# Kernel tuning notes

Hardware: AMD Instinct MI355X
Metric: run time of the kernel (lower is better)

Reference implementation:

```python
import jax, jax.numpy as jnp
import numpy as np

G, R, M, H, NH, OUT = 2048, 1024, 1024, 256, 8, 2
DH = H // NH


def _ln(x, g, b):
    m = jnp.mean(x, -1, keepdims=True)
    v = jnp.var(x, -1, keepdims=True)
    return (x - m) * jax.lax.rsqrt(v + 1e-5) * g + b


def _mha(xq, xkv, w, mask=None):
    # w: [4, H, H] = (Wq, Wk, Wv, Wo); mask: [Nq, Nk] bool (True = attend)
    q = (xq @ w[0]).reshape(-1, NH, DH)
    k = (xkv @ w[1]).reshape(-1, NH, DH)
    v = (xkv @ w[2]).reshape(-1, NH, DH)
    s = jnp.einsum('qhd,khd->hqk', q, k) * np.float32(1.0 / np.sqrt(DH))
    if mask is not None:
        s = jnp.where(mask[None], s, jnp.float32(-1e9))
    a = jax.nn.softmax(s, -1)
    ctx = jnp.einsum('hqk,khd->qhd', a, v).reshape(xq.shape[0], H)
    return ctx @ w[3]


def setup_inputs() -> dict:
    key = jax.random.key(0)
    ks = jax.random.split(key, 32)
    sc = np.float32(1.0 / np.sqrt(H))

    def n(i, shape, s=sc):
        return jax.random.normal(ks[i], shape, jnp.float32) * s

    inp = {}
    inp['gene_emb'] = n(0, (G, H), 0.02)
    inp['reaction_emb'] = n(1, (R, H), 0.02)
    inp['metab_emb'] = n(2, (M, H), 0.02)
    # PreProcessor (note: torch code reuses ONE LayerNorm instance -> shared params)
    inp['pre_w1'] = n(3, (H, H)); inp['pre_b1'] = jnp.zeros((H,), jnp.float32)
    inp['pre_w2'] = n(4, (H, H)); inp['pre_b2'] = jnp.zeros((H,), jnp.float32)
    inp['pre_ln_g'] = jnp.ones((H,), jnp.float32); inp['pre_ln_b'] = jnp.zeros((H,), jnp.float32)
    # NSA: 'M' block = masked attention per edge type (4), 'S' block = full self-attn per node type (3)
    inp['wm'] = n(5, (4, 4, H, H))
    inp['ws'] = n(6, (3, 4, H, H))
    inp['ln_g'] = jnp.ones((3, H), jnp.float32); inp['ln_b'] = jnp.zeros((3, H), jnp.float32)
    # AttentionalGraphAggregation
    inp['gate_w1'] = n(7, (H, H // 2)); inp['gate_b1'] = jnp.zeros((H // 2,), jnp.float32)
    inp['gate_w2'] = n(8, (H // 2, 1)); inp['gate_b2'] = jnp.zeros((1,), jnp.float32)
    inp['tr_w'] = n(9, (H, H)); inp['tr_b'] = jnp.zeros((H,), jnp.float32)
    # prediction head: num_layers=1 -> single Linear
    inp['head_w'] = n(10, (H, OUT)); inp['head_b'] = jnp.zeros((OUT,), jnp.float32)
    # dense edge masks (sparse biological graphs)
    inp['adj_pp'] = jax.random.bernoulli(ks[11], 0.01, (G, G))
    inp['adj_rr'] = jax.random.bernoulli(ks[12], 0.01, (G, G))
    inp['inc_gpr'] = jax.random.bernoulli(ks[13], 0.01, (R, G))
    inp['adj_mm'] = jax.random.bernoulli(ks[14], 0.01, (M, M))
    return inp


def reference(gene_emb, reaction_emb, metab_emb, pre_w1, pre_b1, pre_w2, pre_b2,
              pre_ln_g, pre_ln_b, wm, ws, ln_g, ln_b, gate_w1, gate_b1, gate_w2,
              gate_b2, tr_w, tr_b, head_w, head_b, adj_pp, adj_rr, inc_gpr, adj_mm):
    # preprocessor MLP on gene embeddings (single-graph path; dropout=eval/identity)
    h = jax.nn.relu(_ln(gene_emb @ pre_w1 + pre_b1, pre_ln_g, pre_ln_b))
    xg = jax.nn.relu(_ln(h @ pre_w2 + pre_b2, pre_ln_g, pre_ln_b))
    xr, xm = reaction_emb, metab_emb
    # 'M' block: masked cross/self attention per edge type, sum-aggregated per dst type
    mg = _mha(xg, xg, wm[0], adj_pp) + _mha(xg, xg, wm[1], adj_rr)
    mr = _mha(xr, xg, wm[2], inc_gpr)
    mm = _mha(xm, xm, wm[3], adj_mm)
    xg, xr, xm = xg + mg, xr + mr, xm + mm
    # 'S' block: full self-attention within each node set
    xg = xg + _mha(xg, xg, ws[0])
    xr = xr + _mha(xr, xr, ws[1])
    xm = xm + _mha(xm, xm, ws[2])
    # per-node-type layer norms (gene branch feeds the head)
    xg = _ln(xg, ln_g[0], ln_b[0])
    # attentional graph aggregation over gene nodes (single graph -> plain softmax)
    gate = jax.nn.relu(xg @ gate_w1 + gate_b1) @ gate_w2 + gate_b2  # [G, 1]
    a = jax.nn.softmax(gate, 0)
    t = jax.nn.relu(xg @ tr_w + tr_b)
    pooled = jnp.sum(a * t, 0, keepdims=True)  # [1, H]
    return pooled @ head_w + head_b  # [1, OUT]
```

## Files before the change

kernel.cpp:

```cpp
#include <hip/hip_runtime.h>
#include <hip/hip_bf16.h>
#include <cmath>
#include <cstdint>

typedef unsigned int u32;
typedef unsigned char u8;
typedef unsigned short ushort;
typedef __attribute__((ext_vector_type(8))) short short8;
typedef __attribute__((ext_vector_type(4))) float f32x4;
typedef __attribute__((ext_vector_type(16))) float f32x16;

#define Gn 2048
#define Hd 256

static __device__ __forceinline__ ushort f2bf(float x) {
    __hip_bfloat16 b = __float2bfloat16(x);
    return *reinterpret_cast<ushort*>(&b);
}

__global__ __launch_bounds__(256) void detect2_kernel(const u8* __restrict__ src,
                                                      int* __restrict__ cnt) {
    const int idx = blockIdx.x * 256 + threadIdx.x;
    const uint4 w = ((const uint4*)src)[idx];
    int c0 = ((w.x & 0xffu) ? 1 : 0) + ((w.y & 0xffu) ? 1 : 0) +
             ((w.z & 0xffu) ? 1 : 0) + ((w.w & 0xffu) ? 1 : 0);
    int c1 = ((w.x & 0xffffff00u) ? 1 : 0) + ((w.y & 0xffffff00u) ? 1 : 0) +
             ((w.z & 0xffffff00u) ? 1 : 0) + ((w.w & 0xffffff00u) ? 1 : 0);
    #pragma unroll
    for (int o = 1; o < 64; o <<= 1) { c0 += __shfl_xor(c0, o); c1 += __shfl_xor(c1, o); }
    if ((threadIdx.x & 63) == 0) {
        if (c0) atomicAdd(&cnt[0], c0);
        if (c1) atomicAdd(&cnt[1], c1);
    }
}

__global__ __launch_bounds__(256) void pack_mask_kernel(
    const u8* __restrict__ src, const int* __restrict__ cnt,
    u32* __restrict__ bits, int nwords_per_row, int ncols)
{
    const int idx = blockIdx.x * 256 + threadIdx.x;
    const int row = idx / nwords_per_row;
    const int w = idx - row * nwords_per_row;
    const int f = (cnt[0] > 0) ? ((cnt[1] > 0) ? 1 : 0) : 2;
    u32 v = 0;
    if (f == 1) {
        const uint4* p = (const uint4*)(src + (long)row * ncols + w * 32);
        const uint4 q0 = p[0], q1 = p[1];
        const u32 ws8[8] = {q0.x, q0.y, q0.z, q0.w, q1.x, q1.y, q1.z, q1.w};
        #pragma unroll
        for (int j = 0; j < 8; ++j) {
            const u32 x = ws8[j];
            const u32 m = (((x & 0x7f7f7f7fu) + 0x7f7f7f7fu) | x) & 0x80808080u;
            const u32 b4 = ((m >> 7) & 1u) | ((m >> 14) & 2u) |
                           ((m >> 21) & 4u) | ((m >> 28) & 8u);
            v |= b4 << (j * 4);
        }
    } else if (f == 0) {
        const uint4* p = (const uint4*)((const int*)src + (long)row * ncols + w * 32);
        #pragma unroll
        for (int j = 0; j < 8; ++j) {
            const uint4 q = p[j];
            v |= (q.x ? 1u : 0u) << (j * 4 + 0);
            v |= (q.y ? 1u : 0u) << (j * 4 + 1);
            v |= (q.z ? 1u : 0u) << (j * 4 + 2);
            v |= (q.w ? 1u : 0u) << (j * 4 + 3);
        }
    } else {
        const uint4* p = (const uint4*)((const float*)src + (long)row * ncols + w * 32);
        #pragma unroll
        for (int j = 0; j < 8; ++j) {
            const uint4 q = p[j];
            v |= ((q.x & 0x7fffffffu) ? 1u : 0u) << (j * 4 + 0);
            v |= ((q.y & 0x7fffffffu) ? 1u : 0u) << (j * 4 + 1);
            v |= ((q.z & 0x7fffffffu) ? 1u : 0u) << (j * 4 + 2);
            v |= ((q.w & 0x7fffffffu) ? 1u : 0u) << (j * 4 + 3);
        }
    }
    bits[idx] = v;
}

__global__ __launch_bounds__(256) void preconv_kernel(
    const float* __restrict__ pre_w1, const float* __restrict__ pre_w2,
    const float* __restrict__ wm, const float* __restrict__ wsw,
    const float* __restrict__ gate_w1, const float* __restrict__ tr_w,
    ushort* __restrict__ bt_hi, ushort* __restrict__ bt_lo)
{
    const int slot = blockIdx.x;
    const int k0 = blockIdx.y * 32;
    const float* src; int ncols = 256;
    if (slot == 0) src = pre_w1;
    else if (slot == 1) src = pre_w2;
    else if (slot < 6) src = wm + (long)(slot - 2) * 65536;
    else if (slot < 10) src = wm + (long)(4 + slot - 6) * 65536;
    else if (slot < 14) src = wsw + (long)(slot - 10) * 65536;
    else if (slot == 14) { src = gate_w1; ncols = 128; }
    else src = tr_w;

    __shared__ float T[32][257];
    const int tid = threadIdx.x;
    const int lsh = (ncols == 256) ? 6 : 5;
    const int tot = 32 << lsh;
    for (int i = tid; i < tot; i += 256) {
        const int kk = i >> lsh, c4 = (i & ((1 << lsh) - 1)) << 2;
        const float4 v = *(const float4*)&src[(long)(k0 + kk) * ncols + c4];
        T[kk][c4 + 0] = v.x; T[kk][c4 + 1] = v.y;
        T[kk][c4 + 2] = v.z; T[kk][c4 + 3] = v.w;
    }
    __syncthreads();
    if (tid < ncols) {
        ushort hb[32], lb[32];
        #pragma unroll
        for (int kk = 0; kk < 32; ++kk) {
            const float x = T[kk][tid];
            const u32 bi = __float_as_uint(x);
            const ushort h = (ushort)(bi >> 16);
            const float fh = __uint_as_float(bi & 0xffff0000u);
            hb[kk] = h; lb[kk] = f2bf(x - fh);
        }
        ushort* oh = bt_hi + (long)slot * 65536 + tid * 256 + k0;
        ushort* ol = bt_lo + (long)slot * 65536 + tid * 256 + k0;
        #pragma unroll
        for (int q = 0; q < 4; ++q) {
            *(uint4*)&oh[q * 8] = *(const uint4*)&hb[q * 8];
            *(uint4*)&ol[q * 8] = *(const uint4*)&lb[q * 8];
        }
    }
}

template <int BETA, int RELU, int OUTMODE, int QKVMODE, int KT>
__global__ __launch_bounds__(128) void gemm_mfma_kernel(
    const float* __restrict__ A, int lda,
    const ushort* __restrict__ bt_hi, const ushort* __restrict__ bt_lo,
    int slot0, int slot2, const float* __restrict__ bias,
    float* __restrict__ C, int N)
{
    const int tid = threadIdx.x;
    const int wv = tid >> 6, l = tid & 63;
    const int lr = l & 15, lg = l >> 4;
    const int row = blockIdx.x * 32 + wv * 16 + lr;
    const int col0 = blockIdx.y * 64;
    int slot = slot0, zq = 0, buf = 0;
    if (QKVMODE == 1) {
        const int z = blockIdx.z;
        slot = slot0 + z + z / 3; zq = z % 3; buf = z / 3;
    } else if (QKVMODE == 2) {
        const int z = blockIdx.z;
        slot = slot0 + z; zq = z;
    }
    const ushort* bhb = bt_hi + (long)slot * 65536;
    const ushort* blb = bt_lo + (long)slot * 65536;
    const float* arow = A + (long)row * lda;

    const f32x4 z4 = {0.f, 0.f, 0.f, 0.f};
    f32x4 acc[4] = {z4, z4, z4, z4};

    #pragma unroll
    for (int ks = 0; ks < KT / 32; ++ks) {
        const int k0 = ks * 32;
        const ushort* bh; const ushort* bl;
        if (KT == 512 && k0 >= 256) {
            bh = bt_hi + (long)slot2 * 65536 + (k0 - 256);
            bl = bt_lo + (long)slot2 * 65536 + (k0 - 256);
        } else { bh = bhb + k0; bl = blb + k0; }
        float av[8];
        *(float4*)&av[0] = *(const float4*)&arow[k0 + lg * 8];
        *(float4*)&av[4] = *(const float4*)&arow[k0 + lg * 8 + 4];
        short8 ahi, alo;
        #pragma unroll
        for (int j = 0; j < 8; ++j) {
            const u32 bi = __float_as_uint(av[j]);
            ahi[j] = (short)(bi >> 16);
            const float fh = __uint_as_float(bi & 0xffff0000u);
            alo[j] = (short)f2bf(av[j] - fh);
        }
        #pragma unroll
        for (int f = 0; f < 4; ++f) {
            const long bo = (long)(col0 + f * 16 + lr) * 256 + lg * 8;
            const short8 bhi = *(const short8*)&bh[bo];
            const short8 blo = *(const short8*)&bl[bo];
            acc[f] = __builtin_amdgcn_mfma_f32_16x16x32_bf16(ahi, bhi, acc[f], 0, 0, 0);
            acc[f] = __builtin_amdgcn_mfma_f32_16x16x32_bf16(alo, bhi, acc[f], 0, 0, 0);
            acc[f] = __builtin_amdgcn_mfma_f32_16x16x32_bf16(ahi, blo, acc[f], 0, 0, 0);
        }
    }

    const float QS = 0.17677669529663687f * 1.4426950408889634f;

    #pragma unroll
    for (int f = 0; f < 4; ++f) {
        const int col = col0 + f * 16 + lr;
        const float bv = bias ? bias[col] : 0.f;
        #pragma unroll
        for (int r = 0; r < 4; ++r) {
            const int rr = blockIdx.x * 32 + wv * 16 + lg * 4 + r;
            float v = acc[f][r] + bv;
            if (OUTMODE == 1) {
                if (zq == 0) v *= QS;
                ushort* ob = (ushort*)C + (long)buf * 1572864;
                const int h = col >> 5, d = col & 31;
                if (zq < 2) ob[zq * 524288 + ((h * 2048 + rr) << 5) + d] = f2bf(v);
                else        ob[1048576 + ((h * 32 + d) << 11) + rr] = f2bf(v);
            } else {
                if (BETA) v += C[(long)rr * N + col];
                if (RELU) v = fmaxf(v, 0.f);
                C[(long)rr * N + col] = v;
            }
        }
    }
}

template <int RELU, int DUP>
__global__ __launch_bounds__(64) void ln_kernel(
    const float* __restrict__ X, const float* __restrict__ gw,
    const float* __restrict__ bw, float* __restrict__ Y, float* __restrict__ Y2)
{
    const int row = blockIdx.x, tid = threadIdx.x;
    const float4 x = *(const float4*)&X[(long)row * 256 + (tid << 2)];
    float s = x.x + x.y + x.z + x.w;
    float s2 = x.x * x.x + x.y * x.y + x.z * x.z + x.w * x.w;
    #pragma unroll
    for (int o = 1; o < 64; o <<= 1) { s += __shfl_xor(s, o); s2 += __shfl_xor(s2, o); }
    const float mean = s * (1.f / 256.f);
    const float var = s2 * (1.f / 256.f) - mean * mean;
    const float rs = rsqrtf(var + 1e-5f);
    const float4 g4 = *(const float4*)&gw[tid << 2];
    const float4 b4 = *(const float4*)&bw[tid << 2];
    float4 y;
    y.x = (x.x - mean) * rs * g4.x + b4.x;
    y.y = (x.y - mean) * rs * g4.y + b4.y;
    y.z = (x.z - mean) * rs * g4.z + b4.z;
    y.w = (x.w - mean) * rs * g4.w + b4.w;
    if (RELU) {
        y.x = fmaxf(y.x, 0.f); y.y = fmaxf(y.y, 0.f);
        y.z = fmaxf(y.z, 0.f); y.w = fmaxf(y.w, 0.f);
    }
    *(float4*)&Y[(long)row * 256 + (tid << 2)] = y;
    if (DUP) *(float4*)&Y2[(long)row * 256 + (tid << 2)] = y;
}

template <int MASKED>
__global__ __launch_bounds__(256) void attn_mfma_kernel(
    const ushort* __restrict__ qkvb, const u32* __restrict__ mb0,
    const u32* __restrict__ mb1, float* __restrict__ ctx)
{
    const int zb = blockIdx.z;
    const ushort* qb = qkvb + (long)zb * 1572864;
    const ushort* kb = qb + 524288;
    const ushort* vt = qb + 1048576;
    const u32* maskbits = MASKED ? ((zb == 0) ? mb0 : mb1) : nullptr;
    const int h = blockIdx.x, qt = blockIdx.y;
    const int wv = threadIdx.x >> 6;
    const int l = threadIdx.x & 63;
    const int lq = l & 31;
    const int hi = l >> 5;
    const int qglob = qt * 32 + lq;

    __shared__ float Mm[3][32], Ml[3][32];
    __shared__ float Macc[3][64][16];
    __shared__ float ctile[32][33];

    const int qoff = ((h * 2048 + qglob) << 5) + hi * 8;
    const short8 qf0 = *(const short8*)&qb[qoff];
    const short8 qf1 = *(const short8*)&qb[qoff + 16];

    float m = -INFINITY, lsum = 0.f;
    f32x16 acc, zz16;
    #pragma unroll
    for (int i = 0; i < 16; ++i) { acc[i] = 0.f; zz16[i] = 0.f; }

    const int kt0 = wv * 512;
    #pragma unroll 2
    for (int it = 0; it < 16; ++it) {
        const int kbase = kt0 + it * 32;
        const int koff = ((h * 2048 + kbase + lq) << 5) + hi * 8;
        const short8 kf0 = *(const short8*)&kb[koff];
        const short8 kf1 = *(const short8*)&kb[koff + 16];
        f32x16 s = __builtin_amdgcn_mfma_f32_32x32x16_bf16(kf0, qf0, zz16, 0, 0, 0);
        s = __builtin_amdgcn_mfma_f32_32x32x16_bf16(kf1, qf1, s, 0, 0, 0);
        float sc[16];
        if (MASKED) {
            const u32 mw = maskbits[qglob * 64 + (kbase >> 5)];
            #pragma unroll
            for (int g = 0; g < 4; ++g) {
                const u32 nib = mw >> (8 * g + 4 * hi);
                #pragma unroll
                for (int j = 0; j < 4; ++j)
                    sc[4 * g + j] = ((nib >> j) & 1u) ? s[4 * g + j] : -1e9f;
            }
        } else {
            #pragma unroll
            for (int i = 0; i < 16; ++i) sc[i] = s[i];
        }
        float t[8];
        #pragma unroll
        for (int i = 0; i < 8; ++i) t[i] = fmaxf(sc[i], sc[i + 8]);
        #pragma unroll
        for (int i = 0; i < 4; ++i) t[i] = fmaxf(t[i], t[i + 4]);
        float mt = fmaxf(fmaxf(t[0], t[1]), fmaxf(t[2], t[3]));
        mt = fmaxf(mt, __shfl_xor(mt, 32));
        const float mn = fmaxf(m, mt);
        if (__ballot(mn != m)) {
            const float fac = __builtin_amdgcn_exp2f(m - mn);
            lsum *= fac;
            #pragma unroll
            for (int i = 0; i < 16; ++i) acc[i] *= fac;
            m = mn;
        }
        #pragma unroll
        for (int i = 0; i < 16; ++i) sc[i] = __builtin_amdgcn_exp2f(sc[i] - m);
        #pragma unroll
        for (int i = 0; i < 8; ++i) t[i] = sc[i] + sc[i + 8];
        #pragma unroll
        for (int i = 0; i < 4; ++i) t[i] = t[i] + t[i + 4];
        float ps = (t[0] + t[1]) + (t[2] + t[3]);
        ps += __shfl_xor(ps, 32);
        lsum += ps;
        u32 pk[8];
        #pragma unroll
        for (int g = 0; g < 4; ++g) {
            asm("v_cvt_pk_bf16_f32 %0, %1, %2"
                : "=v"(pk[2 * g]) : "v"(sc[4 * g + 0]), "v"(sc[4 * g + 1]));
            asm("v_cvt_pk_bf16_f32 %0, %1, %2"
                : "=v"(pk[2 * g + 1]) : "v"(sc[4 * g + 2]), "v"(sc[4 * g + 3]));
        }
        asm volatile("v_permlane32_swap_b32 %0, %1" : "+v"(pk[0]), "+v"(pk[2]));
        asm volatile("v_permlane32_swap_b32 %0, %1" : "+v"(pk[1]), "+v"(pk[3]));
        asm volatile("v_permlane32_swap_b32 %0, %1" : "+v"(pk[4]), "+v"(pk[6]));
        asm volatile("v_permlane32_swap_b32 %0, %1" : "+v"(pk[5]), "+v"(pk[7]));
        short8 pB0, pB1;
        ((u32*)&pB0)[0] = pk[0]; ((u32*)&pB0)[1] = pk[1];
        ((u32*)&pB0)[2] = pk[2]; ((u32*)&pB0)[3] = pk[3];
        ((u32*)&pB1)[0] = pk[4]; ((u32*)&pB1)[1] = pk[5];
        ((u32*)&pB1)[2] = pk[6]; ((u32*)&pB1)[3] = pk[7];
        const int voff = ((h * 32 + lq) << 11) + kbase + hi * 8;
        const short8 vf0 = *(const short8*)&vt[voff];
        const short8 vf1 = *(const short8*)&vt[voff + 16];
        acc = __builtin_amdgcn_mfma_f32_32x32x16_bf16(vf0, pB0, acc, 0, 0, 0);
        acc = __builtin_amdgcn_mfma_f32_32x32x16_bf16(vf1, pB1, acc, 0, 0, 0);
    }

    if (wv) {
        if (l < 32) { Mm[wv - 1][l] = m; Ml[wv - 1][l] = lsum; }
        #pragma unroll
        for (int i = 0; i < 16; ++i) Macc[wv - 1][l][i] = acc[i];
    }
    __syncthreads();
    if (wv == 0) {
        float M = m;
        #pragma unroll
        for (int w = 0; w < 3; ++w) M = fmaxf(M, Mm[w][lq]);
        const float f0 = __builtin_amdgcn_exp2f(m - M);
        float den = lsum * f0;
        float o[16];
        #pragma unroll
        for (int i = 0; i < 16; ++i) o[i] = acc[i] * f0;
        #pragma unroll
        for (int w = 0; w < 3; ++w) {
            const float fw = __builtin_amdgcn_exp2f(Mm[w][lq] - M);
            den += Ml[w][lq] * fw;
            #pragma unroll
            for (int i = 0; i < 16; ++i) o[i] += Macc[w][l][i] * fw;
        }
        const float inv = 1.f / den;
        #pragma unroll
        for (int i = 0; i < 16; ++i)
            ctile[(i & 3) + 8 * (i >> 2) + 4 * hi][lq] = o[i] * inv;
    }
    __syncthreads();
    {
        const int t = threadIdx.x;
        const int q = t >> 3, d0 = (t & 7) << 2;
        float4 ov;
        ov.x = ctile[d0 + 0][q]; ov.y = ctile[d0 + 1][q];
        ov.z = ctile[d0 + 2][q]; ov.w = ctile[d0 + 3][q];
        *(float4*)&ctx[(long)(qt * 32 + q) * 512 + zb * 256 + h * 32 + d0] = ov;
    }
}

__global__ __launch_bounds__(256) void gate2_kernel(
    const float* __restrict__ g1, const float* __restrict__ w2,
    const float* __restrict__ b2, float* __restrict__ gv)
{
    int g = blockIdx.x * 256 + threadIdx.x;
    float s = 0.f;
    #pragma unroll
    for (int k = 0; k < 128; k += 4) {
        float4 x = *(const float4*)&g1[(long)g * 128 + k];
        float4 w = *(const float4*)&w2[k];
        s += x.x * w.x + x.y * w.y + x.z * w.z + x.w * w.w;
    }
    gv[g] = s + b2[0];
}

__global__ __launch_bounds__(256) void softmax2048_kernel(float* __restrict__ gv) {
    __shared__ float red[4];
    const int tid = threadIdx.x;
    float v[8];
    float m = -INFINITY;
    #pragma unroll
    for (int i = 0; i < 8; ++i) { v[i] = gv[tid + (i << 8)]; m = fmaxf(m, v[i]); }
    #pragma unroll
    for (int o = 1; o < 64; o <<= 1) m = fmaxf(m, __shfl_xor(m, o));
    if ((tid & 63) == 0) red[tid >> 6] = m;
    __syncthreads();
    m = fmaxf(fmaxf(red[0], red[1]), fmaxf(red[2], red[3]));
    __syncthreads();
    float s = 0.f;
    #pragma unroll
    for (int i = 0; i < 8; ++i) { v[i] = __expf(v[i] - m); s += v[i]; }
    #pragma unroll
    for (int o = 1; o < 64; o <<= 1) s += __shfl_xor(s, o);
    if ((tid & 63) == 0) red[tid >> 6] = s;
    __syncthreads();
    s = red[0] + red[1] + red[2] + red[3];
    const float inv = 1.f / s;
    #pragma unroll
    for (int i = 0; i < 8; ++i) gv[tid + (i << 8)] = v[i] * inv;
}

__global__ __launch_bounds__(256) void wsum_part_kernel(
    const float* __restrict__ a, const float* __restrict__ t,
    float* __restrict__ partial)
{
    const int b = blockIdx.x, col = threadIdx.x;
    const int base = b * 16;
    float s = 0.f;
    #pragma unroll
    for (int i = 0; i < 16; ++i)
        s += a[base + i] * t[(long)(base + i) * 256 + col];
    partial[b * 256 + col] = s;
}

__global__ __launch_bounds__(256) void head2_kernel(
    const float* __restrict__ partial, const float* __restrict__ hw,
    const float* __restrict__ hb, float* __restrict__ out)
{
    __shared__ float red0[4], red1[4];
    const int tid = threadIdx.x;
    float p = 0.f;
    #pragma unroll 8
    for (int b = 0; b < 128; ++b) p += partial[b * 256 + tid];
    float s0 = p * hw[tid * 2 + 0];
    float s1 = p * hw[tid * 2 + 1];
    #pragma unroll
    for (int o = 1; o < 64; o <<= 1) { s0 += __shfl_xor(s0, o); s1 += __shfl_xor(s1, o); }
    if ((tid & 63) == 0) { red0[tid >> 6] = s0; red1[tid >> 6] = s1; }
    __syncthreads();
    if (tid == 0) {
        out[0] = red0[0] + red0[1] + red0[2] + red0[3] + hb[0];
        out[1] = red1[0] + red1[1] + red1[2] + red1[3] + hb[1];
    }
}

extern "C" void kernel_launch(void* const* d_in, const int* in_sizes, int n_in,
                              void* d_out, int out_size, void* d_ws, size_t ws_size,
                              hipStream_t stream)
{
    (void)in_sizes; (void)n_in; (void)out_size; (void)ws_size;
    const float* gene_emb = (const float*)d_in[0];
    const float* pre_w1   = (const float*)d_in[3];
    const float* pre_b1   = (const float*)d_in[4];
    const float* pre_w2   = (const float*)d_in[5];
    const float* pre_b2   = (const float*)d_in[6];
    const float* pre_ln_g = (const float*)d_in[7];
    const float* pre_ln_b = (const float*)d_in[8];
    const float* wm       = (const float*)d_in[9];
    const float* wsw      = (const float*)d_in[10];
    const float* ln_g     = (const float*)d_in[11];
    const float* ln_b     = (const float*)d_in[12];
    const float* gate_w1  = (const float*)d_in[13];
    const float* gate_b1  = (const float*)d_in[14];
    const float* gate_w2  = (const float*)d_in[15];
    const float* gate_b2  = (const float*)d_in[16];
    const float* tr_w     = (const float*)d_in[17];
    const float* tr_b     = (const float*)d_in[18];
    const float* head_w   = (const float*)d_in[19];
    const float* head_b   = (const float*)d_in[20];
    const u8* adj_pp      = (const u8*)d_in[21];
    const u8* adj_rr      = (const u8*)d_in[22];

    const long NHf = (long)Gn * Hd;
    float* tmp0    = (float*)d_ws;
    float* xg      = tmp0 + NHf;
    float* xg1     = xg + NHf;
    float* ctx2    = xg1 + NHf;
    float* g1      = ctx2 + 2 * NHf;
    float* gatev   = g1 + (long)Gn * 128;
    float* partial = gatev + Gn;
    int* cnt       = (int*)(partial + 128 * 256);
    u32* bits_pp   = (u32*)(cnt + 64);
    u32* bits_rr   = bits_pp + (long)Gn * 64;
    ushort* qkvb   = (ushort*)(bits_rr + (long)Gn * 64);
    ushort* bt_hi  = qkvb + 2L * 1572864;
    ushort* bt_lo  = bt_hi + 16L * 65536;

    dim3 B256(256), B64g(2048), T64(64), B128(128);
    dim3 gS(64, 4), gGate(64, 2);

    hipMemsetAsync((void*)cnt, 0, 2 * sizeof(int), stream);
    detect2_kernel<<<dim3(64), B256, 0, stream>>>(adj_pp, cnt);
    pack_mask_kernel<<<dim3(512), B256, 0, stream>>>(adj_pp, cnt, bits_pp, 64, 2048);
    pack_mask_kernel<<<dim3(512), B256, 0, stream>>>(adj_rr, cnt, bits_rr, 64, 2048);
    preconv_kernel<<<dim3(16, 8), B256, 0, stream>>>(pre_w1, pre_w2, wm, wsw,
                                                     gate_w1, tr_w, bt_hi, bt_lo);

    gemm_mfma_kernel<0, 0, 0, 0, 256><<<gS, B128, 0, stream>>>(gene_emb, 256, bt_hi, bt_lo, 0, 0, pre_b1, tmp0, 256);
    ln_kernel<1, 0><<<B64g, T64, 0, stream>>>(tmp0, pre_ln_g, pre_ln_b, xg, nullptr);
    gemm_mfma_kernel<0, 0, 0, 0, 256><<<gS, B128, 0, stream>>>(xg, 256, bt_hi, bt_lo, 1, 0, pre_b2, tmp0, 256);
    ln_kernel<1, 1><<<B64g, T64, 0, stream>>>(tmp0, pre_ln_g, pre_ln_b, xg, xg1);

    gemm_mfma_kernel<0, 0, 1, 1, 256><<<dim3(64, 4, 6), B128, 0, stream>>>(xg, 256, bt_hi, bt_lo, 2, 0, nullptr, (float*)qkvb, 256);
    attn_mfma_kernel<1><<<dim3(8, 64, 2), B256, 0, stream>>>(qkvb, bits_pp, bits_rr, ctx2);
    gemm_mfma_kernel<1, 0, 0, 0, 512><<<gS, B128, 0, stream>>>(ctx2, 512, bt_hi, bt_lo, 5, 9, nullptr, xg1, 256);

    gemm_mfma_kernel<0, 0, 1, 2, 256><<<dim3(64, 4, 3), B128, 0, stream>>>(xg1, 256, bt_hi, bt_lo, 10, 0, nullptr, (float*)qkvb, 256);
    attn_mfma_kernel<0><<<dim3(8, 64, 1), B256, 0, stream>>>(qkvb, nullptr, nullptr, ctx2);
    gemm_mfma_kernel<1, 0, 0, 0, 256><<<gS, B128, 0, stream>>>(ctx2, 512, bt_hi, bt_lo, 13, 0, nullptr, xg1, 256);

    ln_kernel<0, 0><<<B64g, T64, 0, stream>>>(xg1, ln_g, ln_b, xg, nullptr);

    gemm_mfma_kernel<0, 1, 0, 0, 256><<<gGate, B128, 0, stream>>>(xg, 256, bt_hi, bt_lo, 14, 0, gate_b1, g1, 128);
    gate2_kernel<<<dim3(8), B256, 0, stream>>>(g1, gate_w2, gate_b2, gatev);
    softmax2048_kernel<<<dim3(1), B256, 0, stream>>>(gatev);
    gemm_mfma_kernel<0, 1, 0, 0, 256><<<gS, B128, 0, stream>>>(xg, 256, bt_hi, bt_lo, 15, 0, tr_b, tmp0, 256);
    wsum_part_kernel<<<dim3(128), B256, 0, stream>>>(gatev, tmp0, partial);
    head2_kernel<<<dim3(1), B256, 0, stream>>>(partial, head_w, head_b, (float*)d_out);
}
```

Baseline: 229.1 us.

## Replace masked dense attention with CSR sparse attention and retile GEMMs

Masked attention now builds a CSR index from the packed adjacency bits and only visits edges, using an online softmax per row. Empty rows fall back to the mean of V, which matches the -1e9 masking semantics. The dense self-attention gets its own kernel with 8 waves per block. GEMMs move to single-wave 16x32 tiles for more blocks, the gate and transform GEMMs merge into one launch, and the two mask packs merge into one. The sparse path relies on the ~1% edge density and adds CSR build kernels plus irregular gather loads.

```diff
diff --git a/kernel.cpp b/kernel.cpp
--- a/kernel.cpp
+++ b/kernel.cpp
@@ -9,6 +9,7 @@
 typedef __attribute__((ext_vector_type(8))) short short8;
 typedef __attribute__((ext_vector_type(4))) float f32x4;
 typedef __attribute__((ext_vector_type(16))) float f32x16;
+typedef __attribute__((ext_vector_type(4))) unsigned short us4;
 
 #define Gn 2048
 #define Hd 256
@@ -16,6 +17,9 @@
 static __device__ __forceinline__ ushort f2bf(float x) {
     __hip_bfloat16 b = __float2bfloat16(x);
     return *reinterpret_cast<ushort*>(&b);
+}
+static __device__ __forceinline__ float bf2f(ushort u) {
+    return __uint_as_float(((u32)u) << 16);
 }
 
 __global__ __launch_bounds__(256) void detect2_kernel(const u8* __restrict__ src,
@@ -35,16 +39,19 @@
 }
 
 __global__ __launch_bounds__(256) void pack_mask_kernel(
-    const u8* __restrict__ src, const int* __restrict__ cnt,
-    u32* __restrict__ bits, int nwords_per_row, int ncols)
-{
+    const u8* __restrict__ src0, const u8* __restrict__ src1,
+    const int* __restrict__ cnt, u32* __restrict__ bits)
+{
+    const int z = blockIdx.y;
+    const u8* src = z ? src1 : src0;
+    u32* bz = bits + (long)z * 131072;
     const int idx = blockIdx.x * 256 + threadIdx.x;
-    const int row = idx / nwords_per_row;
-    const int w = idx - row * nwords_per_row;
+    const int row = idx >> 6;
+    const int w = idx & 63;
     const int f = (cnt[0] > 0) ? ((cnt[1] > 0) ? 1 : 0) : 2;
     u32 v = 0;
     if (f == 1) {
-        const uint4* p = (const uint4*)(src + (long)row * ncols + w * 32);
+        const uint4* p = (const uint4*)(src + (long)row * 2048 + w * 32);
         const uint4 q0 = p[0], q1 = p[1];
         const u32 ws8[8] = {q0.x, q0.y, q0.z, q0.w, q1.x, q1.y, q1.z, q1.w};
         #pragma unroll
@@ -56,7 +63,7 @@
             v |= b4 << (j * 4);
         }
     } else if (f == 0) {
-        const uint4* p = (const uint4*)((const int*)src + (long)row * ncols + w * 32);
+        const uint4* p = (const uint4*)((const int*)src + (long)row * 2048 + w * 32);
         #pragma unroll
         for (int j = 0; j < 8; ++j) {
             const uint4 q = p[j];
@@ -66,7 +73,7 @@
             v |= (q.w ? 1u : 0u) << (j * 4 + 3);
         }
     } else {
-        const uint4* p = (const uint4*)((const float*)src + (long)row * ncols + w * 32);
+        const uint4* p = (const uint4*)((const float*)src + (long)row * 2048 + w * 32);
         #pragma unroll
         for (int j = 0; j < 8; ++j) {
             const uint4 q = p[j];
@@ -76,7 +83,59 @@
             v |= ((q.w & 0x7fffffffu) ? 1u : 0u) << (j * 4 + 3);
         }
     }
-    bits[idx] = v;
+    bz[idx] = v;
+}
+
+__global__ __launch_bounds__(256) void csr_rowptr_kernel(
+    const u32* __restrict__ bits, int* __restrict__ rowptr)
+{
+    const int z = blockIdx.x;
+    const u32* b = bits + (long)z * 131072;
+    int* rp = rowptr + z * 2049;
+    const int t = threadIdx.x;
+    int d[8]; int tot = 0;
+    #pragma unroll
+    for (int i = 0; i < 8; ++i) {
+        const uint4* p = (const uint4*)&b[(t * 8 + i) * 64];
+        int c = 0;
+        #pragma unroll
+        for (int w = 0; w < 16; ++w) {
+            const uint4 q = p[w];
+            c += __popc(q.x) + __popc(q.y) + __popc(q.z) + __popc(q.w);
+        }
+        d[i] = c; tot += c;
+    }
+    __shared__ int s[256];
+    s[t] = tot; __syncthreads();
+    for (int o = 1; o < 256; o <<= 1) {
+        const int v = (t >= o) ? s[t - o] : 0;
+        __syncthreads();
+        s[t] += v;
+        __syncthreads();
+    }
+    int base = t ? s[t - 1] : 0;
+    #pragma unroll
+    for (int i = 0; i < 8; ++i) { rp[t * 8 + i] = base; base += d[i]; }
+    if (t == 255) rp[2048] = base;
+}
+
+__global__ __launch_bounds__(256) void csr_fill_kernel(
+    const u32* __restrict__ bits, const int* __restrict__ rowptr,
+    int* __restrict__ colidx)
+{
+    const int z = blockIdx.y;
+    const int r = blockIdx.x * 256 + threadIdx.x;
+    const u32* b = bits + (long)z * 131072 + r * 64;
+    int o = rowptr[z * 2049 + r];
+    int* ci = colidx + (long)z * 1048576;
+    for (int w = 0; w < 64; ++w) {
+        u32 x = b[w];
+        while (x) {
+            const int j = __ffs(x) - 1;
+            ci[o++] = w * 32 + j;
+            x &= x - 1;
+        }
+    }
 }
 
 __global__ __launch_bounds__(256) void preconv_kernel(
@@ -128,31 +187,38 @@
 }
 
 template <int BETA, int RELU, int OUTMODE, int QKVMODE, int KT>
-__global__ __launch_bounds__(128) void gemm_mfma_kernel(
+__global__ __launch_bounds__(64) void gemm_mfma_kernel(
     const float* __restrict__ A, int lda,
     const ushort* __restrict__ bt_hi, const ushort* __restrict__ bt_lo,
     int slot0, int slot2, const float* __restrict__ bias,
-    float* __restrict__ C, int N)
-{
-    const int tid = threadIdx.x;
-    const int wv = tid >> 6, l = tid & 63;
+    const float* __restrict__ bias2, float* __restrict__ C,
+    float* __restrict__ C2, int N)
+{
+    const int l = threadIdx.x;
     const int lr = l & 15, lg = l >> 4;
-    const int row = blockIdx.x * 32 + wv * 16 + lr;
-    const int col0 = blockIdx.y * 64;
+    const int row = blockIdx.x * 16 + lr;
+    const int col0 = blockIdx.y * 32;
     int slot = slot0, zq = 0, buf = 0;
+    const float* bp = bias;
+    float* Cp = C;
+    int Nn = N;
     if (QKVMODE == 1) {
         const int z = blockIdx.z;
         slot = slot0 + z + z / 3; zq = z % 3; buf = z / 3;
     } else if (QKVMODE == 2) {
-        const int z = blockIdx.z;
-        slot = slot0 + z; zq = z;
+        slot = slot0 + blockIdx.z; zq = blockIdx.z;
+    } else if (QKVMODE == 3) {
+        if (blockIdx.z == 1) {
+            if (col0 >= 128) return;
+            slot = slot2; bp = bias2; Cp = C2; Nn = 128;
+        }
     }
     const ushort* bhb = bt_hi + (long)slot * 65536;
     const ushort* blb = bt_lo + (long)slot * 65536;
     const float* arow = A + (long)row * lda;
 
     const f32x4 z4 = {0.f, 0.f, 0.f, 0.f};
-    f32x4 acc[4] = {z4, z4, z4, z4};
+    f32x4 acc[2] = {z4, z4};
 
     #pragma unroll
     for (int ks = 0; ks < KT / 32; ++ks) {
@@ -174,7 +240,7 @@
             alo[j] = (short)f2bf(av[j] - fh);
         }
         #pragma unroll
-        for (int f = 0; f < 4; ++f) {
+        for (int f = 0; f < 2; ++f) {
             const long bo = (long)(col0 + f * 16 + lr) * 256 + lg * 8;
             const short8 bhi = *(const short8*)&bh[bo];
             const short8 blo = *(const short8*)&bl[bo];
@@ -187,23 +253,25 @@
     const float QS = 0.17677669529663687f * 1.4426950408889634f;
 
     #pragma unroll
-    for (int f = 0; f < 4; ++f) {
+    for (int f = 0; f < 2; ++f) {
         const int col = col0 + f * 16 + lr;
-        const float bv = bias ? bias[col] : 0.f;
+        const float bv = bp ? bp[col] : 0.f;
         #pragma unroll
         for (int r = 0; r < 4; ++r) {
-            const int rr = blockIdx.x * 32 + wv * 16 + lg * 4 + r;
+            const int rr = blockIdx.x * 16 + lg * 4 + r;
             float v = acc[f][r] + bv;
             if (OUTMODE == 1) {
                 if (zq == 0) v *= QS;
-                ushort* ob = (ushort*)C + (long)buf * 1572864;
+                ushort* ob = (ushort*)Cp + (long)buf * 1572864;
                 const int h = col >> 5, d = col & 31;
-                if (zq < 2) ob[zq * 524288 + ((h * 2048 + rr) << 5) + d] = f2bf(v);
-                else        ob[1048576 + ((h * 32 + d) << 11) + rr] = f2bf(v);
+                if (QKVMODE == 1 || zq < 2)
+                    ob[zq * 524288 + ((h * 2048 + rr) << 5) + d] = f2bf(v);
+                else
+                    ob[1048576 + ((h * 32 + d) << 11) + rr] = f2bf(v);
             } else {
-                if (BETA) v += C[(long)rr * N + col];
+                if (BETA) v += Cp[(long)rr * Nn + col];
                 if (RELU) v = fmaxf(v, 0.f);
-                C[(long)rr * N + col] = v;
+                Cp[(long)rr * Nn + col] = v;
             }
         }
     }
@@ -238,16 +306,86 @@
     if (DUP) *(float4*)&Y2[(long)row * 256 + (tid << 2)] = y;
 }
 
-template <int MASKED>
-__global__ __launch_bounds__(256) void attn_mfma_kernel(
-    const ushort* __restrict__ qkvb, const u32* __restrict__ mb0,
-    const u32* __restrict__ mb1, float* __restrict__ ctx)
-{
-    const int zb = blockIdx.z;
-    const ushort* qb = qkvb + (long)zb * 1572864;
+__global__ __launch_bounds__(256) void vmean_kernel(
+    const ushort* __restrict__ qkvb, float* __restrict__ vmean)
+{
+    const int z = blockIdx.x, h = blockIdx.y;
+    const ushort* vr = qkvb + (long)z * 1572864 + 1048576 + ((long)(h * 2048) << 5);
+    const int t = threadIdx.x;
+    const int d = t & 31, c = t >> 5;
+    float s = 0.f;
+    for (int k = c * 256; k < c * 256 + 256; ++k) s += bf2f(vr[(k << 5) + d]);
+    __shared__ float red[8][32];
+    red[c][d] = s;
+    __syncthreads();
+    if (c == 0) {
+        float tot = 0.f;
+        #pragma unroll
+        for (int i = 0; i < 8; ++i) tot += red[i][d];
+        vmean[z * 256 + h * 32 + d] = tot * (1.f / 2048.f);
+    }
+}
+
+__global__ __launch_bounds__(64) void attn_sparse_kernel(
+    const ushort* __restrict__ qkvb, const int* __restrict__ rowptr,
+    const int* __restrict__ colidx, const float* __restrict__ vmean,
+    float* __restrict__ ctx)
+{
+    const int r = blockIdx.x, z = blockIdx.y;
+    const ushort* qb = qkvb + (long)z * 1572864;
+    const ushort* kb = qb + 524288;
+    const ushort* vr = qb + 1048576;
+    const int l = threadIdx.x;
+    const int h = l >> 3, dg = l & 7;
+    float* orow = &ctx[(long)r * 512 + z * 256 + h * 32 + dg * 4];
+    const int rp0 = rowptr[z * 2049 + r];
+    const int rp1 = rowptr[z * 2049 + r + 1];
+    if (rp0 == rp1) {
+        *(float4*)orow = *(const float4*)&vmean[z * 256 + h * 32 + dg * 4];
+        return;
+    }
+    float q0, q1, q2, q3;
+    {
+        const us4 qv = *(const us4*)&qb[((h * 2048 + r) << 5) + dg * 4];
+        q0 = bf2f(qv[0]); q1 = bf2f(qv[1]); q2 = bf2f(qv[2]); q3 = bf2f(qv[3]);
+    }
+    const int* ci = colidx + (long)z * 1048576;
+    float m = -INFINITY, lsum = 0.f;
+    float a0 = 0.f, a1 = 0.f, a2 = 0.f, a3 = 0.f;
+    int kn = ci[rp0];
+    us4 kv = *(const us4*)&kb[((h * 2048 + kn) << 5) + dg * 4];
+    us4 vv = *(const us4*)&vr[((h * 2048 + kn) << 5) + dg * 4];
+    for (int e = rp0; e < rp1; ++e) {
+        const us4 kc = kv, vc = vv;
+        if (e + 1 < rp1) {
+            kn = ci[e + 1];
+            kv = *(const us4*)&kb[((h * 2048 + kn) << 5) + dg * 4];
+            vv = *(const us4*)&vr[((h * 2048 + kn) << 5) + dg * 4];
+        }
+        float s = q0 * bf2f(kc[0]) + q1 * bf2f(kc[1]) +
+                  q2 * bf2f(kc[2]) + q3 * bf2f(kc[3]);
+        s += __shfl_xor(s, 1); s += __shfl_xor(s, 2); s += __shfl_xor(s, 4);
+        const float mn = fmaxf(m, s);
+        const float fac = __builtin_amdgcn_exp2f(m - mn);
+        const float p = __builtin_amdgcn_exp2f(s - mn);
+        lsum = lsum * fac + p;
+        a0 = a0 * fac + p * bf2f(vc[0]);
+        a1 = a1 * fac + p * bf2f(vc[1]);
+        a2 = a2 * fac + p * bf2f(vc[2]);
+        a3 = a3 * fac + p * bf2f(vc[3]);
+        m = mn;
+    }
+    const float inv = 1.f / lsum;
+    float4 o; o.x = a0 * inv; o.y = a1 * inv; o.z = a2 * inv; o.w = a3 * inv;
+    *(float4*)orow = o;
+}
+
+__global__ __launch_bounds__(512) void attn_dense_kernel(
+    const ushort* __restrict__ qkvb, float* __restrict__ ctx)
+{
+    const ushort* qb = qkvb;
     const ushort* kb = qb + 524288;
     const ushort* vt = qb + 1048576;
-    const u32* maskbits = MASKED ? ((zb == 0) ? mb0 : mb1) : nullptr;
     const int h = blockIdx.x, qt = blockIdx.y;
     const int wv = threadIdx.x >> 6;
     const int l = threadIdx.x & 63;
@@ -255,8 +393,8 @@
     const int hi = l >> 5;
     const int qglob = qt * 32 + lq;
 
-    __shared__ float Mm[3][32], Ml[3][32];
-    __shared__ float Macc[3][64][16];
+    __shared__ float Mm[7][32], Ml[7][32];
+    __shared__ float Macc[7][64][16];
     __shared__ float ctile[32][33];
 
     const int qoff = ((h * 2048 + qglob) << 5) + hi * 8;
@@ -268,9 +406,9 @@
     #pragma unroll
     for (int i = 0; i < 16; ++i) { acc[i] = 0.f; zz16[i] = 0.f; }
 
-    const int kt0 = wv * 512;
+    const int kt0 = wv * 256;
     #pragma unroll 2
-    for (int it = 0; it < 16; ++it) {
+    for (int it = 0; it < 8; ++it) {
         const int kbase = kt0 + it * 32;
         const int koff = ((h * 2048 + kbase + lq) << 5) + hi * 8;
         const short8 kf0 = *(const short8*)&kb[koff];
@@ -278,19 +416,8 @@
         f32x16 s = __builtin_amdgcn_mfma_f32_32x32x16_bf16(kf0, qf0, zz16, 0, 0, 0);
         s = __builtin_amdgcn_mfma_f32_32x32x16_bf16(kf1, qf1, s, 0, 0, 0);
         float sc[16];
-        if (MASKED) {
-            const u32 mw = maskbits[qglob * 64 + (kbase >> 5)];
-            #pragma unroll
-            for (int g = 0; g < 4; ++g) {
-                const u32 nib = mw >> (8 * g + 4 * hi);
-                #pragma unroll
-                for (int j = 0; j < 4; ++j)
-                    sc[4 * g + j] = ((nib >> j) & 1u) ? s[4 * g + j] : -1e9f;
-            }
-        } else {
-            #pragma unroll
-            for (int i = 0; i < 16; ++i) sc[i] = s[i];
-        }
+        #pragma unroll
+        for (int i = 0; i < 16; ++i) sc[i] = s[i];
         float t[8];
         #pragma unroll
         for (int i = 0; i < 8; ++i) t[i] = fmaxf(sc[i], sc[i + 8]);
@@ -348,14 +475,14 @@
     if (wv == 0) {
         float M = m;
         #pragma unroll
-        for (int w = 0; w < 3; ++w) M = fmaxf(M, Mm[w][lq]);
+        for (int w = 0; w < 7; ++w) M = fmaxf(M, Mm[w][lq]);
         const float f0 = __builtin_amdgcn_exp2f(m - M);
         float den = lsum * f0;
         float o[16];
         #pragma unroll
         for (int i = 0; i < 16; ++i) o[i] = acc[i] * f0;
         #pragma unroll
-        for (int w = 0; w < 3; ++w) {
+        for (int w = 0; w < 7; ++w) {
             const float fw = __builtin_amdgcn_exp2f(Mm[w][lq] - M);
             den += Ml[w][lq] * fw;
             #pragma unroll
@@ -367,13 +494,13 @@
             ctile[(i & 3) + 8 * (i >> 2) + 4 * hi][lq] = o[i] * inv;
     }
     __syncthreads();
-    {
+    if (threadIdx.x < 256) {
         const int t = threadIdx.x;
         const int q = t >> 3, d0 = (t & 7) << 2;
         float4 ov;
         ov.x = ctile[d0 + 0][q]; ov.y = ctile[d0 + 1][q];
         ov.z = ctile[d0 + 2][q]; ov.w = ctile[d0 + 3][q];
-        *(float4*)&ctx[(long)(qt * 32 + q) * 512 + zb * 256 + h * 32 + d0] = ov;
+        *(float4*)&ctx[(long)(qt * 32 + q) * 512 + h * 32 + d0] = ov;
     }
 }
 
@@ -487,42 +614,45 @@
     float* g1      = ctx2 + 2 * NHf;
     float* gatev   = g1 + (long)Gn * 128;
     float* partial = gatev + Gn;
-    int* cnt       = (int*)(partial + 128 * 256);
-    u32* bits_pp   = (u32*)(cnt + 64);
-    u32* bits_rr   = bits_pp + (long)Gn * 64;
-    ushort* qkvb   = (ushort*)(bits_rr + (long)Gn * 64);
+    float* vmeanp  = partial + 128 * 256;
+    int* cnt       = (int*)(vmeanp + 512);
+    int* rowptr    = cnt + 64;
+    int* colidx    = rowptr + 4160;
+    u32* bits      = (u32*)(colidx + 2L * 1048576);
+    ushort* qkvb   = (ushort*)(bits + 262144);
     ushort* bt_hi  = qkvb + 2L * 1572864;
     ushort* bt_lo  = bt_hi + 16L * 65536;
 
-    dim3 B256(256), B64g(2048), T64(64), B128(128);
-    dim3 gS(64, 4), gGate(64, 2);
+    dim3 B256(256), B64g(2048), T64(64);
+    dim3 gStd(128, 8);
 
     hipMemsetAsync((void*)cnt, 0, 2 * sizeof(int), stream);
     detect2_kernel<<<dim3(64), B256, 0, stream>>>(adj_pp, cnt);
-    pack_mask_kernel<<<dim3(512), B256, 0, stream>>>(adj_pp, cnt, bits_pp, 64, 2048);
-    pack_mask_kernel<<<dim3(512), B256, 0, stream>>>(adj_rr, cnt, bits_rr, 64, 2048);
+    pack_mask_kernel<<<dim3(512, 2), B256, 0, stream>>>(adj_pp, adj_rr, cnt, bits);
+    csr_rowptr_kernel<<<dim3(2), B256, 0, stream>>>(bits, rowptr);
+    csr_fill_kernel<<<dim3(8, 2), B256, 0, stream>>>(bits, rowptr, colidx);
     preconv_kernel<<<dim3(16, 8), B256, 0, stream>>>(pre_w1, pre_w2, wm, wsw,
                                                      gate_w1, tr_w, bt_hi, bt_lo);
 
-    gemm_mfma_kernel<0, 0, 0, 0, 256><<<gS, B128, 0, stream>>>(gene_emb, 256, bt_hi, bt_lo, 0, 0, pre_b1, tmp0, 256);
+    gemm_mfma_kernel<0, 0, 0, 0, 256><<<gStd, T64, 0, stream>>>(gene_emb, 256, bt_hi, bt_lo, 0, 0, pre_b1, nullptr, tmp0, nullptr, 256);
     ln_kernel<1, 0><<<B64g, T64, 0, stream>>>(tmp0, pre_ln_g, pre_ln_b, xg, nullptr);
-    gemm_mfma_kernel<0, 0, 0, 0, 256><<<gS, B128, 0, stream>>>(xg, 256, bt_hi, bt_lo, 1, 0, pre_b2, tmp0, 256);
+    gemm_mfma_kernel<0, 0, 0, 0, 256><<<gStd, T64, 0, stream>>>(xg, 256, bt_hi, bt_lo, 1, 0, pre_b2, nullptr, tmp0, nullptr, 256);
     ln_kernel<1, 1><<<B64g, T64, 0, stream>>>(tmp0, pre_ln_g, pre_ln_b, xg, xg1);
 
-    gemm_mfma_kernel<0, 0, 1, 1, 256><<<dim3(64, 4, 6), B128, 0, stream>>>(xg, 256, bt_hi, bt_lo, 2, 0, nullptr, (float*)qkvb, 256);
-    attn_mfma_kernel<1><<<dim3(8, 64, 2), B256, 0, stream>>>(qkvb, bits_pp, bits_rr, ctx2);
-    gemm_mfma_kernel<1, 0, 0, 0, 512><<<gS, B128, 0, stream>>>(ctx2, 512, bt_hi, bt_lo, 5, 9, nullptr, xg1, 256);
-
-    gemm_mfma_kernel<0, 0, 1, 2, 256><<<dim3(64, 4, 3), B128, 0, stream>>>(xg1, 256, bt_hi, bt_lo, 10, 0, nullptr, (float*)qkvb, 256);
-    attn_mfma_kernel<0><<<dim3(8, 64, 1), B256, 0, stream>>>(qkvb, nullptr, nullptr, ctx2);
-    gemm_mfma_kernel<1, 0, 0, 0, 256><<<gS, B128, 0, stream>>>(ctx2, 512, bt_hi, bt_lo, 13, 0, nullptr, xg1, 256);
+    gemm_mfma_kernel<0, 0, 1, 1, 256><<<dim3(128, 8, 6), T64, 0, stream>>>(xg, 256, bt_hi, bt_lo, 2, 0, nullptr, nullptr, (float*)qkvb, nullptr, 256);
+    vmean_kernel<<<dim3(2, 8), B256, 0, stream>>>(qkvb, vmeanp);
+    attn_sparse_kernel<<<dim3(2048, 2), T64, 0, stream>>>(qkvb, rowptr, colidx, vmeanp, ctx2);
+    gemm_mfma_kernel<1, 0, 0, 0, 512><<<gStd, T64, 0, stream>>>(ctx2, 512, bt_hi, bt_lo, 5, 9, nullptr, nullptr, xg1, nullptr, 256);
+
+    gemm_mfma_kernel<0, 0, 1, 2, 256><<<dim3(128, 8, 3), T64, 0, stream>>>(xg1, 256, bt_hi, bt_lo, 10, 0, nullptr, nullptr, (float*)qkvb, nullptr, 256);
+    attn_dense_kernel<<<dim3(8, 64), dim3(512), 0, stream>>>(qkvb, ctx2);
+    gemm_mfma_kernel<1, 0, 0, 0, 256><<<gStd, T64, 0, stream>>>(ctx2, 512, bt_hi, bt_lo, 13, 0, nullptr, nullptr, xg1, nullptr, 256);
 
     ln_kernel<0, 0><<<B64g, T64, 0, stream>>>(xg1, ln_g, ln_b, xg, nullptr);
 
-    gemm_mfma_kernel<0, 1, 0, 0, 256><<<gGate, B128, 0, stream>>>(xg, 256, bt_hi, bt_lo, 14, 0, gate_b1, g1, 128);
+    gemm_mfma_kernel<0, 1, 0, 3, 256><<<dim3(128, 8, 2), T64, 0, stream>>>(xg, 256, bt_hi, bt_lo, 15, 14, tr_b, gate_b1, tmp0, g1, 256);
     gate2_kernel<<<dim3(8), B256, 0, stream>>>(g1, gate_w2, gate_b2, gatev);
     softmax2048_kernel<<<dim3(1), B256, 0, stream>>>(gatev);
-    gemm_mfma_kernel<0, 1, 0, 0, 256><<<gS, B128, 0, stream>>>(xg, 256, bt_hi, bt_lo, 15, 0, tr_b, tmp0, 256);
     wsum_part_kernel<<<dim3(128), B256, 0, stream>>>(gatev, tmp0, partial);
     head2_kernel<<<dim3(1), B256, 0, stream>>>(partial, head_w, head_b, (float*)d_out);
 }
```

Result: slower. 243.0 us (+6.0%).
